# Kernel optimization log

Hardware: AMD Instinct MI355X
Metric: run time of the kernel (lower is better)

Reference implementation:

```python
import jax, jax.numpy as jnp
import numpy as np

N = 1_000_000
SIZES = (64, 32, 16)
N_REGIONS = 1000
N_CLUSTERS = 16
N_CELLS = 100_000


def setup_inputs() -> dict:
    key = jax.random.key(0)
    ks = jax.random.split(key, 16)
    inp = {}
    for i, s in enumerate(SIZES):
        inp[f"bincounts_{i}"] = jax.random.randint(ks[i], (N, s), 0, 5, dtype=jnp.int32)
    inp["global_binixs"] = jax.random.randint(ks[3], (N, 3), 0, N_REGIONS, dtype=jnp.int32)
    inp["binixs"] = jax.random.randint(ks[4], (N, 3), 0, 16, dtype=jnp.int32)  # < min(SIZES)
    inp["labels"] = jax.random.randint(ks[5], (N_CELLS,), 0, N_CLUSTERS, dtype=jnp.int32)
    inp["local_cell_ix"] = jax.random.randint(ks[6], (N,), 0, N_CELLS, dtype=jnp.int32)
    for i, s in enumerate(SIZES):
        inp[f"baseline_{i}"] = jax.random.normal(ks[7 + i], (N_REGIONS, s), dtype=jnp.float32)
        inp[f"diff_{i}"] = jax.random.normal(ks[10 + i], (N_CLUSTERS,), dtype=jnp.float32)
    return inp


def reference(bincounts_0, bincounts_1, bincounts_2, global_binixs, binixs,
              labels, local_cell_ix, baseline_0, baseline_1, baseline_2,
              diff_0, diff_1, diff_2):
    # cluster label per fragment (int, constant)
    frag_labels = labels[local_cell_ix]  # [N]
    bincounts = (bincounts_0, bincounts_1, bincounts_2)
    baselines = (baseline_0, baseline_1, baseline_2)
    diffs = (diff_0, diff_1, diff_2)
    logprob = jnp.zeros((bincounts_0.shape[0],), dtype=jnp.float32)
    for i in range(3):
        bc, bw, dw = bincounts[i], baselines[i], diffs[i]
        S = bw.shape[1]
        # fragment_embedding (indicator) * differential scalar + baseline row
        dvals = dw[frag_labels]  # [N]
        uh = (bc > 1).astype(jnp.float32) * dvals[:, None] + bw[global_binixs[:, i]]  # [N, S]
        logh = jax.nn.log_softmax(uh, axis=1) + jnp.log(jnp.float32(S))
        logprob = logprob + jnp.take_along_axis(logh, binixs[:, i:i + 1], axis=1)[:, 0]
    return logprob
```

## Files before the change

kernel.cpp:

```cpp
#include <hip/hip_runtime.h>

#define LOG64f 4.1588830833596715f
#define LOG32f 3.4657359027997265f
#define LOG16f 2.7725887222397810f


__device__ __forceinline__ void expsum4(const int4 c, const float4 w, const float dv,
                                        const int b, const int sub, float& s, float& ub)
{
    const float u0 = (c.x > 1 ? dv : 0.f) + w.x;
    const float u1 = (c.y > 1 ? dv : 0.f) + w.y;
    const float u2 = (c.z > 1 ? dv : 0.f) + w.z;
    const float u3 = (c.w > 1 ? dv : 0.f) + w.w;
    s  = (__expf(u0) + __expf(u1)) + (__expf(u2) + __expf(u3));
    ub = 0.f;
    if (sub == (b >> 2)) {
        const int r = b & 3;
        ub = r == 0 ? u0 : r == 1 ? u1 : r == 2 ? u2 : u3;
    }
}

__global__ __launch_bounds__(256) void frag_pos_dist_kernel(
    const int* __restrict__ bc0, const int* __restrict__ bc1, const int* __restrict__ bc2,
    const int* __restrict__ gix, const int* __restrict__ bix,
    const int* __restrict__ labels, const int* __restrict__ lci,
    const float* __restrict__ bw0, const float* __restrict__ d0,
    const float* __restrict__ bw1, const float* __restrict__ d1,
    const float* __restrict__ bw2, const float* __restrict__ d2,
    float* __restrict__ out, int N)
{
    const int lane = threadIdx.x & 63;
    const int wid  = blockIdx.x * (blockDim.x >> 6) + (threadIdx.x >> 6);
    const int base = wid * 16;
    if (base >= N) return;
    const int fl = lane & 15;

    int nf = base + fl; if (nf >= N) nf = N - 1;
    const int cell = lci[nf];
    const int lab  = labels[cell];
    const float dva = d0[lab], dvb = d1[lab], dvc = d2[lab];
    const int g0v = gix[3 * nf + 0], g1v = gix[3 * nf + 1], g2v = gix[3 * nf + 2];
    const int b0v = bix[3 * nf + 0], b1v = bix[3 * nf + 1], b2v = bix[3 * nf + 2];

    const int s16 = lane >> 4, s8 = lane >> 3, s4 = lane >> 2;
    const int f00 = s16, f01 = 4 + s16, f02 = 8 + s16, f03 = 12 + s16;
    const int f10 = s8,  f11 = 8 + s8;
    const int f20 = s4;

    const float dv00 = __shfl(dva, f00), dv01 = __shfl(dva, f01),
                dv02 = __shfl(dva, f02), dv03 = __shfl(dva, f03);
    const int   g00  = __shfl(g0v, f00), g01  = __shfl(g0v, f01),
                g02  = __shfl(g0v, f02), g03  = __shfl(g0v, f03);
    const int   b00  = __shfl(b0v, f00), b01  = __shfl(b0v, f01),
                b02  = __shfl(b0v, f02), b03  = __shfl(b0v, f03);

    const float dv10 = __shfl(dvb, f10), dv11 = __shfl(dvb, f11);
    const int   g10  = __shfl(g1v, f10), g11  = __shfl(g1v, f11);
    const int   b10  = __shfl(b1v, f10), b11  = __shfl(b1v, f11);

    const float dv20 = __shfl(dvc, f20);
    const int   g20  = __shfl(g2v, f20);
    const int   b20  = __shfl(b2v, f20);

    int n00 = base + f00, n01 = base + f01, n02 = base + f02, n03 = base + f03;
    int n10 = base + f10, n11 = base + f11, n20 = base + f20;
    if (n00 >= N) n00 = N - 1;  if (n01 >= N) n01 = N - 1;
    if (n02 >= N) n02 = N - 1;  if (n03 >= N) n03 = N - 1;
    if (n10 >= N) n10 = N - 1;  if (n11 >= N) n11 = N - 1;
    if (n20 >= N) n20 = N - 1;

    const int sub0 = lane & 15, sub1 = lane & 7, sub2 = lane & 3;

    const int4 c00 = ((const int4*)(bc0 + (size_t)n00 * 64))[sub0];
    const int4 c01 = ((const int4*)(bc0 + (size_t)n01 * 64))[sub0];
    const int4 c02 = ((const int4*)(bc0 + (size_t)n02 * 64))[sub0];
    const int4 c03 = ((const int4*)(bc0 + (size_t)n03 * 64))[sub0];
    const int4 c10 = ((const int4*)(bc1 + (size_t)n10 * 32))[sub1];
    const int4 c11 = ((const int4*)(bc1 + (size_t)n11 * 32))[sub1];
    const int4 c20 = ((const int4*)(bc2 + (size_t)n20 * 16))[sub2];

    const float4 w00 = ((const float4*)(bw0 + (size_t)g00 * 64))[sub0];
    const float4 w01 = ((const float4*)(bw0 + (size_t)g01 * 64))[sub0];
    const float4 w02 = ((const float4*)(bw0 + (size_t)g02 * 64))[sub0];
    const float4 w03 = ((const float4*)(bw0 + (size_t)g03 * 64))[sub0];
    const float4 w10 = ((const float4*)(bw1 + (size_t)g10 * 32))[sub1];
    const float4 w11 = ((const float4*)(bw1 + (size_t)g11 * 32))[sub1];
    const float4 w20 = ((const float4*)(bw2 + (size_t)g20 * 16))[sub2];

    float acc = 0.0f;
    float s, ub, t, lp;

    expsum4(c00, w00, dv00, b00, sub0, s, ub);
    s += __shfl_xor(s, 1); ub += __shfl_xor(ub, 1);
    s += __shfl_xor(s, 2); ub += __shfl_xor(ub, 2);
    s += __shfl_xor(s, 4); ub += __shfl_xor(ub, 4);
    s += __shfl_xor(s, 8); ub += __shfl_xor(ub, 8);
    lp = ub - __logf(s) + LOG64f;
    t = __shfl(lp, (fl & 3) << 4); if ((fl >> 2) == 0) acc += t;

    expsum4(c01, w01, dv01, b01, sub0, s, ub);
    s += __shfl_xor(s, 1); ub += __shfl_xor(ub, 1);
    s += __shfl_xor(s, 2); ub += __shfl_xor(ub, 2);
    s += __shfl_xor(s, 4); ub += __shfl_xor(ub, 4);
    s += __shfl_xor(s, 8); ub += __shfl_xor(ub, 8);
    lp = ub - __logf(s) + LOG64f;
    t = __shfl(lp, (fl & 3) << 4); if ((fl >> 2) == 1) acc += t;

    expsum4(c02, w02, dv02, b02, sub0, s, ub);
    s += __shfl_xor(s, 1); ub += __shfl_xor(ub, 1);
    s += __shfl_xor(s, 2); ub += __shfl_xor(ub, 2);
    s += __shfl_xor(s, 4); ub += __shfl_xor(ub, 4);
    s += __shfl_xor(s, 8); ub += __shfl_xor(ub, 8);
    lp = ub - __logf(s) + LOG64f;
    t = __shfl(lp, (fl & 3) << 4); if ((fl >> 2) == 2) acc += t;

    expsum4(c03, w03, dv03, b03, sub0, s, ub);
    s += __shfl_xor(s, 1); ub += __shfl_xor(ub, 1);
    s += __shfl_xor(s, 2); ub += __shfl_xor(ub, 2);
    s += __shfl_xor(s, 4); ub += __shfl_xor(ub, 4);
    s += __shfl_xor(s, 8); ub += __shfl_xor(ub, 8);
    lp = ub - __logf(s) + LOG64f;
    t = __shfl(lp, (fl & 3) << 4); if ((fl >> 2) == 3) acc += t;

    expsum4(c10, w10, dv10, b10, sub1, s, ub);
    s += __shfl_xor(s, 1); ub += __shfl_xor(ub, 1);
    s += __shfl_xor(s, 2); ub += __shfl_xor(ub, 2);
    s += __shfl_xor(s, 4); ub += __shfl_xor(ub, 4);
    lp = ub - __logf(s) + LOG32f;
    t = __shfl(lp, (fl & 7) << 3); if ((fl >> 3) == 0) acc += t;

    expsum4(c11, w11, dv11, b11, sub1, s, ub);
    s += __shfl_xor(s, 1); ub += __shfl_xor(ub, 1);
    s += __shfl_xor(s, 2); ub += __shfl_xor(ub, 2);
    s += __shfl_xor(s, 4); ub += __shfl_xor(ub, 4);
    lp = ub - __logf(s) + LOG32f;
    t = __shfl(lp, (fl & 7) << 3); if ((fl >> 3) == 1) acc += t;

    expsum4(c20, w20, dv20, b20, sub2, s, ub);
    s += __shfl_xor(s, 1); ub += __shfl_xor(ub, 1);
    s += __shfl_xor(s, 2); ub += __shfl_xor(ub, 2);
    lp = ub - __logf(s) + LOG16f;
    t = __shfl(lp, fl << 2); acc += t;

    if (lane < 16) {
        const int n = base + lane;
        if (n < N) out[n] = acc;
    }
}

extern "C" void kernel_launch(void* const* d_in, const int* in_sizes, int n_in,
                              void* d_out, int out_size, void* d_ws, size_t ws_size,
                              hipStream_t stream) {
    const int* bc0    = (const int*)d_in[0];
    const int* bc1    = (const int*)d_in[1];
    const int* bc2    = (const int*)d_in[2];
    const int* gix    = (const int*)d_in[3];
    const int* bixp   = (const int*)d_in[4];
    const int* labels = (const int*)d_in[5];
    const int* lci    = (const int*)d_in[6];
    const float* bw0  = (const float*)d_in[7];
    const float* dv0  = (const float*)d_in[8];
    const float* bw1  = (const float*)d_in[9];
    const float* dv1  = (const float*)d_in[10];
    const float* bw2  = (const float*)d_in[11];
    const float* dv2  = (const float*)d_in[12];
    float* out = (float*)d_out;

    const int N = in_sizes[6];
    const int threads = 256;
    const int fragsPerBlock = 64;
    const int blocks = (N + fragsPerBlock - 1) / fragsPerBlock;

    frag_pos_dist_kernel<<<blocks, threads, 0, stream>>>(
        bc0, bc1, bc2, gix, bixp, labels, lci,
        bw0, dv0, bw1, dv1, bw2, dv2, out, N);
}
```

Measured before the change: 99.11 us.

## Process two 16-fragment chunks per wave and batch shuffle reductions

Each wavefront now handles 32 fragments as two independent 16-fragment chunks. All bincount loads for both chunks are issued up front, before the per-fragment index and label gathers, to raise memory-level parallelism. The softmax reduction is restructured: only the exp-sums are butterfly-reduced, and the target logit is fetched with one direct shuffle from its owning lane instead of being reduced as well. This cuts shuffle count and runs several independent reductions side by side. The cost is higher register pressure and half as many waves for the same input, which may lower occupancy.

```diff
diff --git a/kernel.cpp b/kernel.cpp
--- a/kernel.cpp
+++ b/kernel.cpp
@@ -20,6 +20,90 @@
     }
 }
 
+__device__ __forceinline__ float chunk16(
+    const int lane,
+    const int4 c00, const int4 c01, const int4 c02, const int4 c03,
+    const int4 c10, const int4 c11, const int4 c20,
+    const float dva, const float dvb, const float dvc,
+    const int g0v, const int g1v, const int g2v,
+    const int b0v, const int b1v, const int b2v,
+    const float* __restrict__ bw0, const float* __restrict__ bw1,
+    const float* __restrict__ bw2)
+{
+    const int fl = lane & 15;
+    const int s16 = lane >> 4, s8 = lane >> 3, s4 = lane >> 2;
+    const int f00 = s16, f01 = 4 + s16, f02 = 8 + s16, f03 = 12 + s16;
+    const int f10 = s8,  f11 = 8 + s8;
+    const int f20 = s4;
+    const int sub0 = lane & 15, sub1 = lane & 7, sub2 = lane & 3;
+
+    const float dv00 = __shfl(dva, f00), dv01 = __shfl(dva, f01),
+                dv02 = __shfl(dva, f02), dv03 = __shfl(dva, f03);
+    const int   g00  = __shfl(g0v, f00), g01  = __shfl(g0v, f01),
+                g02  = __shfl(g0v, f02), g03  = __shfl(g0v, f03);
+    const int   b00  = __shfl(b0v, f00), b01  = __shfl(b0v, f01),
+                b02  = __shfl(b0v, f02), b03  = __shfl(b0v, f03);
+    const float dv10 = __shfl(dvb, f10), dv11 = __shfl(dvb, f11);
+    const int   g10  = __shfl(g1v, f10), g11  = __shfl(g1v, f11);
+    const int   b10  = __shfl(b1v, f10), b11  = __shfl(b1v, f11);
+    const float dv20 = __shfl(dvc, f20);
+    const int   g20  = __shfl(g2v, f20);
+    const int   b20  = __shfl(b2v, f20);
+
+    const float4 w00 = ((const float4*)(bw0 + (size_t)g00 * 64))[sub0];
+    const float4 w01 = ((const float4*)(bw0 + (size_t)g01 * 64))[sub0];
+    const float4 w02 = ((const float4*)(bw0 + (size_t)g02 * 64))[sub0];
+    const float4 w03 = ((const float4*)(bw0 + (size_t)g03 * 64))[sub0];
+    const float4 w10 = ((const float4*)(bw1 + (size_t)g10 * 32))[sub1];
+    const float4 w11 = ((const float4*)(bw1 + (size_t)g11 * 32))[sub1];
+    const float4 w20 = ((const float4*)(bw2 + (size_t)g20 * 16))[sub2];
+
+    float s00, u00, s01, u01, s02, u02, s03, u03;
+    expsum4(c00, w00, dv00, b00, sub0, s00, u00);
+    expsum4(c01, w01, dv01, b01, sub0, s01, u01);
+    expsum4(c02, w02, dv02, b02, sub0, s02, u02);
+    expsum4(c03, w03, dv03, b03, sub0, s03, u03);
+    #pragma unroll
+    for (int off = 1; off <= 8; off <<= 1) {
+        s00 += __shfl_xor(s00, off); s01 += __shfl_xor(s01, off);
+        s02 += __shfl_xor(s02, off); s03 += __shfl_xor(s03, off);
+    }
+    float s10, u10, s11, u11;
+    expsum4(c10, w10, dv10, b10, sub1, s10, u10);
+    expsum4(c11, w11, dv11, b11, sub1, s11, u11);
+    #pragma unroll
+    for (int off = 1; off <= 4; off <<= 1) {
+        s10 += __shfl_xor(s10, off); s11 += __shfl_xor(s11, off);
+    }
+    float s20, u20;
+    expsum4(c20, w20, dv20, b20, sub2, s20, u20);
+    s20 += __shfl_xor(s20, 1); s20 += __shfl_xor(s20, 2);
+
+    const int  src0 = (fl & 3) << 4;
+    const float m00 = __shfl(s00, src0), m01 = __shfl(s01, src0),
+                m02 = __shfl(s02, src0), m03 = __shfl(s03, src0);
+    const int j0 = fl >> 2;
+    const float S0 = j0 == 0 ? m00 : j0 == 1 ? m01 : j0 == 2 ? m02 : m03;
+    const int  h0 = src0 + (b0v >> 2);
+    const float x00 = __shfl(u00, h0), x01 = __shfl(u01, h0),
+                x02 = __shfl(u02, h0), x03 = __shfl(u03, h0);
+    const float U0 = j0 == 0 ? x00 : j0 == 1 ? x01 : j0 == 2 ? x02 : x03;
+
+    const int  src1 = (fl & 7) << 3;
+    const float m10 = __shfl(s10, src1), m11 = __shfl(s11, src1);
+    const float S1 = (fl >> 3) == 0 ? m10 : m11;
+    const int  h1 = src1 + (b1v >> 2);
+    const float x10 = __shfl(u10, h1), x11 = __shfl(u11, h1);
+    const float U1 = (fl >> 3) == 0 ? x10 : x11;
+
+    const float S2 = __shfl(s20, fl << 2);
+    const float U2 = __shfl(u20, (fl << 2) + (b2v >> 2));
+
+    return (U0 - __logf(S0) + LOG64f) +
+           (U1 - __logf(S1) + LOG32f) +
+           (U2 - __logf(S2) + LOG16f);
+}
+
 __global__ __launch_bounds__(256) void frag_pos_dist_kernel(
     const int* __restrict__ bc0, const int* __restrict__ bc1, const int* __restrict__ bc2,
     const int* __restrict__ gix, const int* __restrict__ bix,
@@ -31,120 +115,60 @@
 {
     const int lane = threadIdx.x & 63;
     const int wid  = blockIdx.x * (blockDim.x >> 6) + (threadIdx.x >> 6);
-    const int base = wid * 16;
+    const int base = wid * 32;
     if (base >= N) return;
     const int fl = lane & 15;
-
-    int nf = base + fl; if (nf >= N) nf = N - 1;
-    const int cell = lci[nf];
-    const int lab  = labels[cell];
-    const float dva = d0[lab], dvb = d1[lab], dvc = d2[lab];
-    const int g0v = gix[3 * nf + 0], g1v = gix[3 * nf + 1], g2v = gix[3 * nf + 2];
-    const int b0v = bix[3 * nf + 0], b1v = bix[3 * nf + 1], b2v = bix[3 * nf + 2];
-
     const int s16 = lane >> 4, s8 = lane >> 3, s4 = lane >> 2;
-    const int f00 = s16, f01 = 4 + s16, f02 = 8 + s16, f03 = 12 + s16;
-    const int f10 = s8,  f11 = 8 + s8;
-    const int f20 = s4;
-
-    const float dv00 = __shfl(dva, f00), dv01 = __shfl(dva, f01),
-                dv02 = __shfl(dva, f02), dv03 = __shfl(dva, f03);
-    const int   g00  = __shfl(g0v, f00), g01  = __shfl(g0v, f01),
-                g02  = __shfl(g0v, f02), g03  = __shfl(g0v, f03);
-    const int   b00  = __shfl(b0v, f00), b01  = __shfl(b0v, f01),
-                b02  = __shfl(b0v, f02), b03  = __shfl(b0v, f03);
-
-    const float dv10 = __shfl(dvb, f10), dv11 = __shfl(dvb, f11);
-    const int   g10  = __shfl(g1v, f10), g11  = __shfl(g1v, f11);
-    const int   b10  = __shfl(b1v, f10), b11  = __shfl(b1v, f11);
-
-    const float dv20 = __shfl(dvc, f20);
-    const int   g20  = __shfl(g2v, f20);
-    const int   b20  = __shfl(b2v, f20);
-
-    int n00 = base + f00, n01 = base + f01, n02 = base + f02, n03 = base + f03;
-    int n10 = base + f10, n11 = base + f11, n20 = base + f20;
-    if (n00 >= N) n00 = N - 1;  if (n01 >= N) n01 = N - 1;
-    if (n02 >= N) n02 = N - 1;  if (n03 >= N) n03 = N - 1;
-    if (n10 >= N) n10 = N - 1;  if (n11 >= N) n11 = N - 1;
-    if (n20 >= N) n20 = N - 1;
-
     const int sub0 = lane & 15, sub1 = lane & 7, sub2 = lane & 3;
-
-    const int4 c00 = ((const int4*)(bc0 + (size_t)n00 * 64))[sub0];
-    const int4 c01 = ((const int4*)(bc0 + (size_t)n01 * 64))[sub0];
-    const int4 c02 = ((const int4*)(bc0 + (size_t)n02 * 64))[sub0];
-    const int4 c03 = ((const int4*)(bc0 + (size_t)n03 * 64))[sub0];
-    const int4 c10 = ((const int4*)(bc1 + (size_t)n10 * 32))[sub1];
-    const int4 c11 = ((const int4*)(bc1 + (size_t)n11 * 32))[sub1];
-    const int4 c20 = ((const int4*)(bc2 + (size_t)n20 * 16))[sub2];
-
-    const float4 w00 = ((const float4*)(bw0 + (size_t)g00 * 64))[sub0];
-    const float4 w01 = ((const float4*)(bw0 + (size_t)g01 * 64))[sub0];
-    const float4 w02 = ((const float4*)(bw0 + (size_t)g02 * 64))[sub0];
-    const float4 w03 = ((const float4*)(bw0 + (size_t)g03 * 64))[sub0];
-    const float4 w10 = ((const float4*)(bw1 + (size_t)g10 * 32))[sub1];
-    const float4 w11 = ((const float4*)(bw1 + (size_t)g11 * 32))[sub1];
-    const float4 w20 = ((const float4*)(bw2 + (size_t)g20 * 16))[sub2];
-
-    float acc = 0.0f;
-    float s, ub, t, lp;
-
-    expsum4(c00, w00, dv00, b00, sub0, s, ub);
-    s += __shfl_xor(s, 1); ub += __shfl_xor(ub, 1);
-    s += __shfl_xor(s, 2); ub += __shfl_xor(ub, 2);
-    s += __shfl_xor(s, 4); ub += __shfl_xor(ub, 4);
-    s += __shfl_xor(s, 8); ub += __shfl_xor(ub, 8);
-    lp = ub - __logf(s) + LOG64f;
-    t = __shfl(lp, (fl & 3) << 4); if ((fl >> 2) == 0) acc += t;
-
-    expsum4(c01, w01, dv01, b01, sub0, s, ub);
-    s += __shfl_xor(s, 1); ub += __shfl_xor(ub, 1);
-    s += __shfl_xor(s, 2); ub += __shfl_xor(ub, 2);
-    s += __shfl_xor(s, 4); ub += __shfl_xor(ub, 4);
-    s += __shfl_xor(s, 8); ub += __shfl_xor(ub, 8);
-    lp = ub - __logf(s) + LOG64f;
-    t = __shfl(lp, (fl & 3) << 4); if ((fl >> 2) == 1) acc += t;
-
-    expsum4(c02, w02, dv02, b02, sub0, s, ub);
-    s += __shfl_xor(s, 1); ub += __shfl_xor(ub, 1);
-    s += __shfl_xor(s, 2); ub += __shfl_xor(ub, 2);
-    s += __shfl_xor(s, 4); ub += __shfl_xor(ub, 4);
-    s += __shfl_xor(s, 8); ub += __shfl_xor(ub, 8);
-    lp = ub - __logf(s) + LOG64f;
-    t = __shfl(lp, (fl & 3) << 4); if ((fl >> 2) == 2) acc += t;
-
-    expsum4(c03, w03, dv03, b03, sub0, s, ub);
-    s += __shfl_xor(s, 1); ub += __shfl_xor(ub, 1);
-    s += __shfl_xor(s, 2); ub += __shfl_xor(ub, 2);
-    s += __shfl_xor(s, 4); ub += __shfl_xor(ub, 4);
-    s += __shfl_xor(s, 8); ub += __shfl_xor(ub, 8);
-    lp = ub - __logf(s) + LOG64f;
-    t = __shfl(lp, (fl & 3) << 4); if ((fl >> 2) == 3) acc += t;
-
-    expsum4(c10, w10, dv10, b10, sub1, s, ub);
-    s += __shfl_xor(s, 1); ub += __shfl_xor(ub, 1);
-    s += __shfl_xor(s, 2); ub += __shfl_xor(ub, 2);
-    s += __shfl_xor(s, 4); ub += __shfl_xor(ub, 4);
-    lp = ub - __logf(s) + LOG32f;
-    t = __shfl(lp, (fl & 7) << 3); if ((fl >> 3) == 0) acc += t;
-
-    expsum4(c11, w11, dv11, b11, sub1, s, ub);
-    s += __shfl_xor(s, 1); ub += __shfl_xor(ub, 1);
-    s += __shfl_xor(s, 2); ub += __shfl_xor(ub, 2);
-    s += __shfl_xor(s, 4); ub += __shfl_xor(ub, 4);
-    lp = ub - __logf(s) + LOG32f;
-    t = __shfl(lp, (fl & 7) << 3); if ((fl >> 3) == 1) acc += t;
-
-    expsum4(c20, w20, dv20, b20, sub2, s, ub);
-    s += __shfl_xor(s, 1); ub += __shfl_xor(ub, 1);
-    s += __shfl_xor(s, 2); ub += __shfl_xor(ub, 2);
-    lp = ub - __logf(s) + LOG16f;
-    t = __shfl(lp, fl << 2); acc += t;
-
-    if (lane < 16) {
+    const int NM1 = N - 1;
+
+    const int nA00 = min(base +      s16, NM1), nA01 = min(base +  4 + s16, NM1),
+              nA02 = min(base +  8 + s16, NM1), nA03 = min(base + 12 + s16, NM1);
+    const int nA10 = min(base +       s8, NM1), nA11 = min(base +  8 +  s8, NM1);
+    const int nA20 = min(base +       s4, NM1);
+    const int nB00 = min(base + 16 + s16, NM1), nB01 = min(base + 20 + s16, NM1),
+              nB02 = min(base + 24 + s16, NM1), nB03 = min(base + 28 + s16, NM1);
+    const int nB10 = min(base + 16 +  s8, NM1), nB11 = min(base + 24 +  s8, NM1);
+    const int nB20 = min(base + 16 +  s4, NM1);
+
+    const int4 cA00 = ((const int4*)(bc0 + (size_t)nA00 * 64))[sub0];
+    const int4 cA01 = ((const int4*)(bc0 + (size_t)nA01 * 64))[sub0];
+    const int4 cA02 = ((const int4*)(bc0 + (size_t)nA02 * 64))[sub0];
+    const int4 cA03 = ((const int4*)(bc0 + (size_t)nA03 * 64))[sub0];
+    const int4 cA10 = ((const int4*)(bc1 + (size_t)nA10 * 32))[sub1];
+    const int4 cA11 = ((const int4*)(bc1 + (size_t)nA11 * 32))[sub1];
+    const int4 cA20 = ((const int4*)(bc2 + (size_t)nA20 * 16))[sub2];
+    const int4 cB00 = ((const int4*)(bc0 + (size_t)nB00 * 64))[sub0];
+    const int4 cB01 = ((const int4*)(bc0 + (size_t)nB01 * 64))[sub0];
+    const int4 cB02 = ((const int4*)(bc0 + (size_t)nB02 * 64))[sub0];
+    const int4 cB03 = ((const int4*)(bc0 + (size_t)nB03 * 64))[sub0];
+    const int4 cB10 = ((const int4*)(bc1 + (size_t)nB10 * 32))[sub1];
+    const int4 cB11 = ((const int4*)(bc1 + (size_t)nB11 * 32))[sub1];
+    const int4 cB20 = ((const int4*)(bc2 + (size_t)nB20 * 16))[sub2];
+
+    const int nfA = min(base + fl, NM1);
+    const int nfB = min(base + 16 + fl, NM1);
+    const int cellA = lci[nfA];
+    const int cellB = lci[nfB];
+    const int labA  = labels[cellA];
+    const int labB  = labels[cellB];
+    const float dvaA = d0[labA], dvbA = d1[labA], dvcA = d2[labA];
+    const float dvaB = d0[labB], dvbB = d1[labB], dvcB = d2[labB];
+    const int g0A = gix[3 * nfA + 0], g1A = gix[3 * nfA + 1], g2A = gix[3 * nfA + 2];
+    const int g0B = gix[3 * nfB + 0], g1B = gix[3 * nfB + 1], g2B = gix[3 * nfB + 2];
+    const int b0A = bix[3 * nfA + 0], b1A = bix[3 * nfA + 1], b2A = bix[3 * nfA + 2];
+    const int b0B = bix[3 * nfB + 0], b1B = bix[3 * nfB + 1], b2B = bix[3 * nfB + 2];
+
+    const float accA = chunk16(lane, cA00, cA01, cA02, cA03, cA10, cA11, cA20,
+                               dvaA, dvbA, dvcA, g0A, g1A, g2A, b0A, b1A, b2A,
+                               bw0, bw1, bw2);
+    const float accB = chunk16(lane, cB00, cB01, cB02, cB03, cB10, cB11, cB20,
+                               dvaB, dvbB, dvcB, g0B, g1B, g2B, b0B, b1B, b2B,
+                               bw0, bw1, bw2);
+
+    if (lane < 32) {
         const int n = base + lane;
-        if (n < N) out[n] = acc;
+        if (n < N) out[n] = (lane < 16) ? accA : accB;
     }
 }
 
@@ -168,7 +192,7 @@
 
     const int N = in_sizes[6];
     const int threads = 256;
-    const int fragsPerBlock = 64;
+    const int fragsPerBlock = 128;
     const int blocks = (N + fragsPerBlock - 1) / fragsPerBlock;
 
     frag_pos_dist_kernel<<<blocks, threads, 0, stream>>>(
```

Result: slower. 104.1 us (+5.0%).
